# Performance work log

Hardware: AMD Instinct MI355X
Metric: run time of the kernel (lower is better)

The kernel has to match this reference:

```python
import jax, jax.numpy as jnp
import numpy as np

SEQ_LEN = 96
D_MODEL = 512
BATCH = 512
FREQ = SEQ_LEN // 2 + 1  # 49
EPS = 1e-5


def setup_inputs() -> dict:
    key = jax.random.key(0)
    ks = jax.random.split(key, 9)
    s = 1.0 / np.sqrt(D_MODEL)
    return {
        "x": jax.random.normal(ks[0], (BATCH, SEQ_LEN, D_MODEL), jnp.float32),
        "freq_weights": jnp.ones((FREQ,), jnp.float32),
        "Wl": jax.random.normal(ks[1], (D_MODEL, D_MODEL), jnp.float32) * s,
        "bl": jax.random.normal(ks[2], (D_MODEL,), jnp.float32) * s,
        "Wh": jax.random.normal(ks[3], (D_MODEL, D_MODEL), jnp.float32) * s,
        "bh": jax.random.normal(ks[4], (D_MODEL,), jnp.float32) * s,
        "Wg": jax.random.normal(ks[5], (2 * D_MODEL, D_MODEL), jnp.float32) * s,
        "bg": jax.random.normal(ks[6], (D_MODEL,), jnp.float32) * s,
        "gamma": jnp.ones((D_MODEL,), jnp.float32),
        "beta": jnp.zeros((D_MODEL,), jnp.float32),
    }


def reference(x, freq_weights, Wl, bl, Wh, bh, Wg, bg, gamma, beta):
    # Batched rfft over seq axis for all channels at once: [B, F, D] complex
    xf = jnp.fft.rfft(x, axis=1)
    xw = xf * freq_weights[None, :, None]
    cutoff = FREQ // 3  # 16 (static)
    idx = jnp.arange(FREQ)[None, :, None]
    x_low_f = jnp.where(idx < cutoff, xw, 0)
    x_high_f = jnp.where(idx >= cutoff, xw, 0)
    x_low = jnp.fft.irfft(x_low_f, n=SEQ_LEN, axis=1)   # [B, S, D]
    x_high = jnp.fft.irfft(x_high_f, n=SEQ_LEN, axis=1)
    x_low = jnp.einsum("bsd,de->bse", x_low, Wl) + bl
    x_high = jnp.einsum("bsd,de->bse", x_high, Wh) + bh
    gate_in = jnp.concatenate([x_low, x_high], axis=-1)  # [B, S, 2D]
    gate = jax.nn.sigmoid(jnp.einsum("bsd,de->bse", gate_in, Wg) + bg)
    out = gate * x_low + (1.0 - gate) * x_high
    y = x + out  # dropout is identity in eval mode
    mu = jnp.mean(y, axis=-1, keepdims=True)
    var = jnp.var(y, axis=-1, keepdims=True)
    return (y - mu) / jnp.sqrt(var + EPS) * gamma + beta
```

## Files before the change

kernel.cpp:

```cpp
#include <hip/hip_runtime.h>

typedef unsigned short u16;
typedef unsigned int u32;

#define SEQ 96
#define DM 512
#define NBATCH 512
#define NFREQ 49
#define CUT 16
#define MROWS (NBATCH * SEQ)

typedef __attribute__((ext_vector_type(8))) short bf16x8;
typedef __attribute__((ext_vector_type(8))) unsigned short u16x8;
typedef __attribute__((ext_vector_type(4))) float f32x4;

__device__ __forceinline__ u16 f2bf(float f) {
  u32 u = __float_as_uint(f);
  u32 r = (u + 0x7fffu + ((u >> 16) & 1u)) >> 16;
  return (u16)r;
}
__device__ __forceinline__ float bf2f(u16 u) {
  return __uint_as_float(((u32)u) << 16);
}

__device__ __forceinline__ void g2l16(const void* g, void* l) {
  __builtin_amdgcn_global_load_lds(
      (const __attribute__((address_space(1))) void*)g,
      (__attribute__((address_space(3))) void*)l, 16, 0, 0);
}

__global__ void build_filters_k(const float* __restrict__ w,
                                u16* __restrict__ FlB, u16* __restrict__ FhB) {
  int idx = blockIdx.x * 256 + threadIdx.x;
  if (idx >= SEQ * SEQ) return;
  int s = idx / SEQ, t = idx % SEQ;
  int d = s - t;
  const float scale = 1.0f / (float)SEQ;
  const float w0 = 6.283185307179586f / (float)SEQ;
  float cl = 0.f, ch = 0.f;
  for (int k = 0; k < NFREQ; k++) {
    int m = (k * d) % SEQ;
    if (m < 0) m += SEQ;
    float c = (k == 0 || k == SEQ / 2) ? 1.0f : 2.0f;
    float v = c * w[k] * cosf(w0 * (float)m) * scale;
    if (k < CUT) cl += v; else ch += v;
  }
  FlB[idx] = f2bf(cl);
  FhB[idx] = f2bf(ch);
}

__global__ void __launch_bounds__(256) transpose_w_k(
    const float* __restrict__ W, u16* __restrict__ Wt, int K, int N) {
  __shared__ float t[32][33];
  int k0 = blockIdx.x * 32, n0 = blockIdx.y * 32;
  int tx = threadIdx.x & 31, ty = threadIdx.x >> 5;
  #pragma unroll
  for (int r = 0; r < 32; r += 8)
    t[ty + r][tx] = W[(size_t)(k0 + ty + r) * N + n0 + tx];
  __syncthreads();
  #pragma unroll
  for (int r = 0; r < 32; r += 8)
    Wt[(size_t)(n0 + ty + r) * K + k0 + tx] = f2bf(t[tx][ty + r]);
}

__global__ void __launch_bounds__(256) filter_fused_k(
    const float* __restrict__ x, const u16* __restrict__ FlB,
    const u16* __restrict__ FhB, u16* __restrict__ xl, u16* __restrict__ xh) {
  __shared__ __align__(16) u16 Bs[128 * SEQ];
  __shared__ __align__(16) u16 As0[2 * SEQ * SEQ];
  __shared__ float xs[SEQ * 33];
  int tid = threadIdx.x;
  int lane = tid & 63, w = tid >> 6;
  int b = blockIdx.x, d0 = blockIdx.y * 128;

  #pragma unroll
  for (int it = 0; it < 9; it++) {
    int c = it * 256 + tid;
    const u16* src = (c < 1152) ? (FlB + c * 8) : (FhB + (c - 1152) * 8);
    g2l16(src, (char*)As0 + ((it * 256 + w * 64) << 4));
  }

  const float* xb = x + (size_t)b * SEQ * DM + d0;
  u32* BsW = (u32*)Bs;
  #pragma unroll
  for (int q = 0; q < 4; q++) {
    #pragma unroll
    for (int v = 0; v < 3; v++) {
      int c = v * 256 + tid;
      int t = c >> 3, f = (c & 7) << 2;
      float4 fv = *(const float4*)(xb + (size_t)t * DM + q * 32 + f);
      xs[t * 33 + f + 0] = fv.x;
      xs[t * 33 + f + 1] = fv.y;
      xs[t * 33 + f + 2] = fv.z;
      xs[t * 33 + f + 3] = fv.w;
    }
    __syncthreads();
    #pragma unroll
    for (int v = 0; v < 6; v++) {
      int c = v * 256 + tid;
      int dl = c / 48, tw = c % 48;
      u32 lo = (u32)f2bf(xs[(2 * tw) * 33 + dl]);
      u32 hi = (u32)f2bf(xs[(2 * tw + 1) * 33 + dl]);
      BsW[(size_t)(q * 32 + dl) * 48 + tw] = lo | (hi << 16);
    }
    __syncthreads();
  }

  const int l15 = lane & 15, lq = lane >> 4;
  f32x4 acc[2][6][2] = {};
  #pragma unroll
  for (int ks = 0; ks < 3; ks++) {
    int kt = ks * 32;
    bf16x8 bfr[2];
    #pragma unroll
    for (int j = 0; j < 2; j++)
      bfr[j] = *(const bf16x8*)&Bs[(w * 32 + j * 16 + l15) * SEQ + kt + lq * 8];
    #pragma unroll
    for (int f = 0; f < 2; f++)
      #pragma unroll
      for (int i = 0; i < 6; i++) {
        bf16x8 afr = *(const bf16x8*)&As0[f * SEQ * SEQ + (i * 16 + l15) * SEQ + kt + lq * 8];
        #pragma unroll
        for (int j = 0; j < 2; j++)
          acc[f][i][j] = __builtin_amdgcn_mfma_f32_16x16x32_bf16(afr, bfr[j], acc[f][i][j], 0, 0, 0);
      }
  }
  #pragma unroll
  for (int f = 0; f < 2; f++) {
    u16* dst = f ? xh : xl;
    #pragma unroll
    for (int i = 0; i < 6; i++)
      #pragma unroll
      for (int j = 0; j < 2; j++) {
        int d = d0 + w * 32 + j * 16 + l15;
        #pragma unroll
        for (int r = 0; r < 4; r++) {
          int s = i * 16 + lq * 4 + r;
          dst[((size_t)b * SEQ + s) * DM + d] = f2bf(acc[f][i][j][r]);
        }
      }
  }
}

__global__ void __launch_bounds__(256) gemm_proj_mfma_k(
    const u16* __restrict__ xl, const u16* __restrict__ xh,
    const u16* __restrict__ Wlt, const u16* __restrict__ Wht,
    const float* __restrict__ bl, const float* __restrict__ bh,
    u16* __restrict__ yl, u16* __restrict__ yh) {
  const u16* A = blockIdx.z ? xh : xl;
  const u16* Bt = blockIdx.z ? Wht : Wlt;
  const float* bias = blockIdx.z ? bh : bl;
  u16* C = blockIdx.z ? yh : yl;

  __shared__ __align__(16) u16 As[128 * 32];
  __shared__ __align__(16) u16 Bs[128 * 32];
  const int m0 = blockIdx.x * 128;
  const int n0 = blockIdx.y * 128;
  const int tid = threadIdx.x;
  const int lane = tid & 63;
  const int w = tid >> 6;
  const int wm = w & 1, wn = w >> 1;
  const int l15 = lane & 15;
  const int lq = lane >> 4;

  f32x4 acc[4][4] = {};

  for (int kt = 0; kt < 512; kt += 32) {
    #pragma unroll
    for (int r = 0; r < 2; r++) {
      int chunk = r * 256 + tid;
      int row = chunk >> 2;
      int ce = (chunk & 3) << 3;
      u32 lo = (u32)((r * 256 + w * 64) << 4);
      g2l16(A + (size_t)(m0 + row) * 512 + kt + ce, (char*)As + lo);
      g2l16(Bt + (size_t)(n0 + row) * 512 + kt + ce, (char*)Bs + lo);
    }
    __syncthreads();
    bf16x8 af[4], bf[4];
    #pragma unroll
    for (int i = 0; i < 4; i++)
      af[i] = *(const bf16x8*)&As[(wm * 64 + i * 16 + l15) * 32 + lq * 8];
    #pragma unroll
    for (int j = 0; j < 4; j++)
      bf[j] = *(const bf16x8*)&Bs[(wn * 64 + j * 16 + l15) * 32 + lq * 8];
    #pragma unroll
    for (int i = 0; i < 4; i++)
      #pragma unroll
      for (int j = 0; j < 4; j++)
        acc[i][j] = __builtin_amdgcn_mfma_f32_16x16x32_bf16(af[i], bf[j], acc[i][j], 0, 0, 0);
    __syncthreads();
  }

  #pragma unroll
  for (int j = 0; j < 4; j++) {
    int n = n0 + wn * 64 + j * 16 + l15;
    float bv = bias[n];
    #pragma unroll
    for (int i = 0; i < 4; i++) {
      int mrow = m0 + wm * 64 + i * 16 + lq * 4;
      #pragma unroll
      for (int r = 0; r < 4; r++)
        C[(size_t)(mrow + r) * 512 + n] = f2bf(acc[i][j][r] + bv);
    }
  }
}

__global__ void __launch_bounds__(256) gemm_gate_mfma_k(
    const u16* __restrict__ yl, const u16* __restrict__ yh,
    const u16* __restrict__ Wgt, const float* __restrict__ bg,
    u16* __restrict__ g) {
  __shared__ __align__(16) u16 As[128 * 32];
  __shared__ __align__(16) u16 Bs[128 * 32];
  const int m0 = blockIdx.x * 128;
  const int n0 = blockIdx.y * 128;
  const int tid = threadIdx.x;
  const int lane = tid & 63;
  const int w = tid >> 6;
  const int wm = w & 1, wn = w >> 1;
  const int l15 = lane & 15;
  const int lq = lane >> 4;

  f32x4 acc[4][4] = {};

  for (int kt = 0; kt < 1024; kt += 32) {
    const u16* Ak = (kt < 512) ? yl : yh;
    int ka = kt & 511;
    #pragma unroll
    for (int r = 0; r < 2; r++) {
      int chunk = r * 256 + tid;
      int row = chunk >> 2;
      int ce = (chunk & 3) << 3;
      u32 lo = (u32)((r * 256 + w * 64) << 4);
      g2l16(Ak + (size_t)(m0 + row) * 512 + ka + ce, (char*)As + lo);
      g2l16(Wgt + (size_t)(n0 + row) * 1024 + kt + ce, (char*)Bs + lo);
    }
    __syncthreads();
    bf16x8 af[4], bf[4];
    #pragma unroll
    for (int i = 0; i < 4; i++)
      af[i] = *(const bf16x8*)&As[(wm * 64 + i * 16 + l15) * 32 + lq * 8];
    #pragma unroll
    for (int j = 0; j < 4; j++)
      bf[j] = *(const bf16x8*)&Bs[(wn * 64 + j * 16 + l15) * 32 + lq * 8];
    #pragma unroll
    for (int i = 0; i < 4; i++)
      #pragma unroll
      for (int j = 0; j < 4; j++)
        acc[i][j] = __builtin_amdgcn_mfma_f32_16x16x32_bf16(af[i], bf[j], acc[i][j], 0, 0, 0);
    __syncthreads();
  }

  #pragma unroll
  for (int j = 0; j < 4; j++) {
    int n = n0 + wn * 64 + j * 16 + l15;
    float bv = bg[n];
    #pragma unroll
    for (int i = 0; i < 4; i++) {
      int mrow = m0 + wm * 64 + i * 16 + lq * 4;
      #pragma unroll
      for (int r = 0; r < 4; r++) {
        float z = acc[i][j][r] + bv;
        g[(size_t)(mrow + r) * 512 + n] = f2bf(1.0f / (1.0f + __expf(-z)));
      }
    }
  }
}

__global__ void __launch_bounds__(256) final_ln_k(
    const float* __restrict__ x, const u16* __restrict__ yl,
    const u16* __restrict__ yh, const u16* __restrict__ g,
    const float* __restrict__ gamma, const float* __restrict__ beta,
    float* __restrict__ out) {
  const int wave = threadIdx.x >> 6;
  const int lane = threadIdx.x & 63;
  const size_t row = (size_t)blockIdx.x * 4 + wave;
  const size_t base = row * 512 + lane * 8;
  const int e = lane * 8;

  float4 xv0 = *(const float4*)(x + base);
  float4 xv1 = *(const float4*)(x + base + 4);
  u16x8 lv = *(const u16x8*)(yl + base);
  u16x8 hv = *(const u16x8*)(yh + base);
  u16x8 gv = *(const u16x8*)(g + base);

  float v[8];
  const float xs[8] = {xv0.x, xv0.y, xv0.z, xv0.w, xv1.x, xv1.y, xv1.z, xv1.w};
  float sum = 0.f, sumsq = 0.f;
  #pragma unroll
  for (int k = 0; k < 8; k++) {
    float gl = bf2f(gv[k]);
    float vv = xs[k] + gl * bf2f(lv[k]) + (1.f - gl) * bf2f(hv[k]);
    v[k] = vv;
    sum += vv;
    sumsq += vv * vv;
  }
  #pragma unroll
  for (int off = 32; off; off >>= 1) {
    sum += __shfl_xor(sum, off);
    sumsq += __shfl_xor(sumsq, off);
  }
  const float mu = sum * (1.f / 512.f);
  const float var = sumsq * (1.f / 512.f) - mu * mu;
  const float inv = rsqrtf(var + 1e-5f);

  float4 gm0 = *(const float4*)(gamma + e);
  float4 gm1 = *(const float4*)(gamma + e + 4);
  float4 bt0 = *(const float4*)(beta + e);
  float4 bt1 = *(const float4*)(beta + e + 4);
  float4 o0, o1;
  o0.x = (v[0] - mu) * inv * gm0.x + bt0.x;
  o0.y = (v[1] - mu) * inv * gm0.y + bt0.y;
  o0.z = (v[2] - mu) * inv * gm0.z + bt0.z;
  o0.w = (v[3] - mu) * inv * gm0.w + bt0.w;
  o1.x = (v[4] - mu) * inv * gm1.x + bt1.x;
  o1.y = (v[5] - mu) * inv * gm1.y + bt1.y;
  o1.z = (v[6] - mu) * inv * gm1.z + bt1.z;
  o1.w = (v[7] - mu) * inv * gm1.w + bt1.w;
  *(float4*)(out + base) = o0;
  *(float4*)(out + base + 4) = o1;
}

extern "C" void kernel_launch(void* const* d_in, const int* in_sizes, int n_in,
                              void* d_out, int out_size, void* d_ws, size_t ws_size,
                              hipStream_t stream) {
  const float* x     = (const float*)d_in[0];
  const float* fw    = (const float*)d_in[1];
  const float* Wl    = (const float*)d_in[2];
  const float* bl    = (const float*)d_in[3];
  const float* Wh    = (const float*)d_in[4];
  const float* bh    = (const float*)d_in[5];
  const float* Wg    = (const float*)d_in[6];
  const float* bg    = (const float*)d_in[7];
  const float* gamma = (const float*)d_in[8];
  const float* beta  = (const float*)d_in[9];
  float* out = (float*)d_out;

  char* ws = (char*)d_ws;
  u16* FlB = (u16*)ws;
  u16* FhB = FlB + SEQ * SEQ;
  u16* Wlt = (u16*)(ws + 64 * 1024);
  u16* Wht = Wlt + 512 * 512;
  u16* Wgt = Wht + 512 * 512;
  size_t tsz = (size_t)MROWS * 512;
  u16* xl = (u16*)(ws + 4 * 1024 * 1024);
  u16* xh = xl + tsz;
  u16* yl = xh + tsz;
  u16* yh = yl + tsz;
  u16* gbuf = xl;

  build_filters_k<<<dim3(36), dim3(256), 0, stream>>>(fw, FlB, FhB);
  transpose_w_k<<<dim3(16, 16), dim3(256), 0, stream>>>(Wl, Wlt, 512, 512);
  transpose_w_k<<<dim3(16, 16), dim3(256), 0, stream>>>(Wh, Wht, 512, 512);
  transpose_w_k<<<dim3(32, 16), dim3(256), 0, stream>>>(Wg, Wgt, 1024, 512);
  filter_fused_k<<<dim3(NBATCH, DM / 128), dim3(256), 0, stream>>>(x, FlB, FhB, xl, xh);
  gemm_proj_mfma_k<<<dim3(MROWS / 128, 4, 2), dim3(256), 0, stream>>>(
      xl, xh, Wlt, Wht, bl, bh, yl, yh);
  gemm_gate_mfma_k<<<dim3(MROWS / 128, 4), dim3(256), 0, stream>>>(yl, yh, Wgt, bg, gbuf);
  final_ln_k<<<dim3(MROWS / 4), dim3(256), 0, stream>>>(x, yl, yh, gbuf, gamma, beta, out);
}
```

Before: 441.5 us.

## Fold projection weights into gate weights and fuse projection and gate GEMMs

Precomputes a combined gate weight Wgc = [Wl·Wg_top; Wh·Wg_bot] and a combined bias b2, so the gate pre-activation can be computed directly from xl/xh instead of from yl/yh. A single 512-thread kernel then runs two groups of waves over the same A tiles: one group produces yl and yh, the other produces the sigmoid gate. This drops the separate gate GEMM and its re-read of yl/yh, and shares the A loads across both. In exchange it adds small weight-prep kernels, extra workspace, a K=1024 loop per block, and extra bf16 rounding in the composed weights. The fused path only runs when the workspace is large enough, otherwise the old two-GEMM path is kept.

Result: slower. 571.8 us (+29.5%).

```diff
diff --git a/kernel.cpp b/kernel.cpp
--- a/kernel.cpp
+++ b/kernel.cpp
@@ -50,17 +50,92 @@
 }
 
 __global__ void __launch_bounds__(256) transpose_w_k(
-    const float* __restrict__ W, u16* __restrict__ Wt, int K, int N) {
+    const float* __restrict__ W, u16* __restrict__ Wt, int K, int N,
+    u16* __restrict__ WB) {
   __shared__ float t[32][33];
   int k0 = blockIdx.x * 32, n0 = blockIdx.y * 32;
   int tx = threadIdx.x & 31, ty = threadIdx.x >> 5;
   #pragma unroll
-  for (int r = 0; r < 32; r += 8)
-    t[ty + r][tx] = W[(size_t)(k0 + ty + r) * N + n0 + tx];
+  for (int r = 0; r < 32; r += 8) {
+    float v = W[(size_t)(k0 + ty + r) * N + n0 + tx];
+    t[ty + r][tx] = v;
+    if (WB) WB[(size_t)(k0 + ty + r) * N + n0 + tx] = f2bf(v);
+  }
   __syncthreads();
   #pragma unroll
   for (int r = 0; r < 32; r += 8)
     Wt[(size_t)(n0 + ty + r) * K + k0 + tx] = f2bf(t[tx][ty + r]);
+}
+
+__global__ void __launch_bounds__(256) wgc_build_k(
+    const u16* __restrict__ Wgt, const u16* __restrict__ WlB,
+    const u16* __restrict__ WhB, u16* __restrict__ Wgc) {
+  __shared__ __align__(16) u16 As[128 * 32];
+  __shared__ __align__(16) u16 Bs[128 * 32];
+  const int n0 = blockIdx.x * 128;
+  const int k0 = blockIdx.y * 128;
+  const int zoff = blockIdx.z ? 512 : 0;
+  const u16* WB = blockIdx.z ? WhB : WlB;
+  const int tid = threadIdx.x;
+  const int lane = tid & 63;
+  const int w = tid >> 6;
+  const int wm = w & 1, wn = w >> 1;
+  const int l15 = lane & 15;
+  const int lq = lane >> 4;
+
+  f32x4 acc[4][4] = {};
+
+  for (int kt = 0; kt < 512; kt += 32) {
+    #pragma unroll
+    for (int r = 0; r < 2; r++) {
+      int chunk = r * 256 + tid;
+      int row = chunk >> 2;
+      int ce = (chunk & 3) << 3;
+      u32 lo = (u32)((r * 256 + w * 64) << 4);
+      g2l16(Wgt + (size_t)(n0 + row) * 1024 + zoff + kt + ce, (char*)As + lo);
+      g2l16(WB + (size_t)(k0 + row) * 512 + kt + ce, (char*)Bs + lo);
+    }
+    __syncthreads();
+    bf16x8 af[4], bf[4];
+    #pragma unroll
+    for (int i = 0; i < 4; i++)
+      af[i] = *(const bf16x8*)&As[(wm * 64 + i * 16 + l15) * 32 + lq * 8];
+    #pragma unroll
+    for (int j = 0; j < 4; j++)
+      bf[j] = *(const bf16x8*)&Bs[(wn * 64 + j * 16 + l15) * 32 + lq * 8];
+    #pragma unroll
+    for (int i = 0; i < 4; i++)
+      #pragma unroll
+      for (int j = 0; j < 4; j++)
+        acc[i][j] = __builtin_amdgcn_mfma_f32_16x16x32_bf16(af[i], bf[j], acc[i][j], 0, 0, 0);
+    __syncthreads();
+  }
+
+  #pragma unroll
+  for (int j = 0; j < 4; j++) {
+    int kcol = k0 + wn * 64 + j * 16 + l15;
+    #pragma unroll
+    for (int i = 0; i < 4; i++) {
+      int nrow = n0 + wm * 64 + i * 16 + lq * 4;
+      #pragma unroll
+      for (int r = 0; r < 4; r++)
+        Wgc[(size_t)(nrow + r) * 1024 + zoff + kcol] = f2bf(acc[i][j][r]);
+    }
+  }
+}
+
+__global__ void __launch_bounds__(256) b2_k(
+    const float* __restrict__ Wg, const float* __restrict__ bl,
+    const float* __restrict__ bh, const float* __restrict__ bg,
+    float* __restrict__ b2) {
+  int n = blockIdx.x * 256 + threadIdx.x;
+  float s = bg[n];
+  #pragma unroll 4
+  for (int e = 0; e < 512; e++) {
+    s += bl[e] * Wg[(size_t)e * 512 + n];
+    s += bh[e] * Wg[(size_t)(512 + e) * 512 + n];
+  }
+  b2[n] = s;
 }
 
 __global__ void __launch_bounds__(256) filter_fused_k(
@@ -139,6 +214,104 @@
           dst[((size_t)b * SEQ + s) * DM + d] = f2bf(acc[f][i][j][r]);
         }
       }
+  }
+}
+
+__global__ void __launch_bounds__(512) fused_pg_k(
+    const u16* __restrict__ xl, const u16* __restrict__ xh,
+    const u16* __restrict__ Wlt, const u16* __restrict__ Wht,
+    const u16* __restrict__ Wgc,
+    const float* __restrict__ bl, const float* __restrict__ bh,
+    const float* __restrict__ b2,
+    u16* __restrict__ yl, u16* __restrict__ yh, u16* __restrict__ g) {
+  __shared__ __align__(16) u16 As[128 * 32];
+  __shared__ __align__(16) u16 By[128 * 32];
+  __shared__ __align__(16) u16 Bz[128 * 32];
+  const int m0 = blockIdx.x * 128;
+  const int n0 = blockIdx.y * 128;
+  const int tid = threadIdx.x;
+  const int lane = tid & 63;
+  const int w = tid >> 6;
+  const bool isY = (w < 4);
+  const int wz = w & 3;
+  const int wm = wz & 1, wn = wz >> 1;
+  const int l15 = lane & 15;
+  const int lq = lane >> 4;
+  const f32x4 fzero = {0.f, 0.f, 0.f, 0.f};
+
+  const int rowS = tid >> 2;
+  const int ce = (tid & 3) << 3;
+  const u32 ldsoff = (u32)((w * 64) << 4);
+
+  f32x4 acc[4][4] = {};
+
+  for (int kt = 0; kt < 1024; kt += 32) {
+    const u16* Asrc = (kt < 512) ? xl : xh;
+    const u16* Bysrc = (kt < 512) ? Wlt : Wht;
+    const int ka = kt & 511;
+    g2l16(Asrc + (size_t)(m0 + rowS) * 512 + ka + ce, (char*)As + ldsoff);
+    g2l16(Bysrc + (size_t)(n0 + rowS) * 512 + ka + ce, (char*)By + ldsoff);
+    g2l16(Wgc + (size_t)(n0 + rowS) * 1024 + kt + ce, (char*)Bz + ldsoff);
+    __syncthreads();
+    const u16* Bsel = isY ? By : Bz;
+    bf16x8 af[4], bf[4];
+    #pragma unroll
+    for (int i = 0; i < 4; i++)
+      af[i] = *(const bf16x8*)&As[(wm * 64 + i * 16 + l15) * 32 + lq * 8];
+    #pragma unroll
+    for (int j = 0; j < 4; j++)
+      bf[j] = *(const bf16x8*)&Bsel[(wn * 64 + j * 16 + l15) * 32 + lq * 8];
+    #pragma unroll
+    for (int i = 0; i < 4; i++)
+      #pragma unroll
+      for (int j = 0; j < 4; j++)
+        acc[i][j] = __builtin_amdgcn_mfma_f32_16x16x32_bf16(af[i], bf[j], acc[i][j], 0, 0, 0);
+    if (kt == 480 && isY) {
+      #pragma unroll
+      for (int j = 0; j < 4; j++) {
+        int n = n0 + wn * 64 + j * 16 + l15;
+        float bv = bl[n];
+        #pragma unroll
+        for (int i = 0; i < 4; i++) {
+          int mrow = m0 + wm * 64 + i * 16 + lq * 4;
+          #pragma unroll
+          for (int r = 0; r < 4; r++)
+            yl[(size_t)(mrow + r) * 512 + n] = f2bf(acc[i][j][r] + bv);
+          acc[i][j] = fzero;
+        }
+      }
+    }
+    __syncthreads();
+  }
+
+  if (isY) {
+    #pragma unroll
+    for (int j = 0; j < 4; j++) {
+      int n = n0 + wn * 64 + j * 16 + l15;
+      float bv = bh[n];
+      #pragma unroll
+      for (int i = 0; i < 4; i++) {
+        int mrow = m0 + wm * 64 + i * 16 + lq * 4;
+        #pragma unroll
+        for (int r = 0; r < 4; r++)
+          yh[(size_t)(mrow + r) * 512 + n] = f2bf(acc[i][j][r] + bv);
+      }
+    }
+  } else {
+    #pragma unroll
+    for (int j = 0; j < 4; j++) {
+      int n = n0 + wn * 64 + j * 16 + l15;
+      float bv = b2[n];
+      #pragma unroll
+      for (int i = 0; i < 4; i++) {
+        int mrow = m0 + wm * 64 + i * 16 + lq * 4;
+        #pragma unroll
+        for (int r = 0; r < 4; r++) {
+          float z = acc[i][j][r] + bv;
+          g[(size_t)(mrow + r) * 512 + n] = f2bf(1.0f / (1.0f + __expf(-z)));
+        }
+      }
+    }
   }
 }
 
@@ -341,20 +514,38 @@
   u16* Wlt = (u16*)(ws + 64 * 1024);
   u16* Wht = Wlt + 512 * 512;
   u16* Wgt = Wht + 512 * 512;
+  u16* WlB = Wgt + 512 * 1024;
+  u16* WhB = WlB + 512 * 512;
+  u16* Wgc = WhB + 512 * 512;
+  float* b2 = (float*)(ws + 6 * 1024 * 1024);
   size_t tsz = (size_t)MROWS * 512;
-  u16* xl = (u16*)(ws + 4 * 1024 * 1024);
+  u16* xl = (u16*)(ws + 8 * 1024 * 1024);
   u16* xh = xl + tsz;
   u16* yl = xh + tsz;
   u16* yh = yl + tsz;
-  u16* gbuf = xl;
+
+  const bool fused = ws_size >= (size_t)8 * 1024 * 1024 + 5 * tsz * sizeof(u16);
+  u16* gbuf = fused ? (yh + tsz) : xl;
 
   build_filters_k<<<dim3(36), dim3(256), 0, stream>>>(fw, FlB, FhB);
-  transpose_w_k<<<dim3(16, 16), dim3(256), 0, stream>>>(Wl, Wlt, 512, 512);
-  transpose_w_k<<<dim3(16, 16), dim3(256), 0, stream>>>(Wh, Wht, 512, 512);
-  transpose_w_k<<<dim3(32, 16), dim3(256), 0, stream>>>(Wg, Wgt, 1024, 512);
+  transpose_w_k<<<dim3(16, 16), dim3(256), 0, stream>>>(Wl, Wlt, 512, 512,
+                                                        fused ? WlB : nullptr);
+  transpose_w_k<<<dim3(16, 16), dim3(256), 0, stream>>>(Wh, Wht, 512, 512,
+                                                        fused ? WhB : nullptr);
+  transpose_w_k<<<dim3(32, 16), dim3(256), 0, stream>>>(Wg, Wgt, 1024, 512, nullptr);
   filter_fused_k<<<dim3(NBATCH, DM / 128), dim3(256), 0, stream>>>(x, FlB, FhB, xl, xh);
-  gemm_proj_mfma_k<<<dim3(MROWS / 128, 4, 2), dim3(256), 0, stream>>>(
-      xl, xh, Wlt, Wht, bl, bh, yl, yh);
-  gemm_gate_mfma_k<<<dim3(MROWS / 128, 4), dim3(256), 0, stream>>>(yl, yh, Wgt, bg, gbuf);
-  final_ln_k<<<dim3(MROWS / 4), dim3(256), 0, stream>>>(x, yl, yh, gbuf, gamma, beta, out);
-}
+
+  if (fused) {
+    wgc_build_k<<<dim3(4, 4, 2), dim3(256), 0, stream>>>(Wgt, WlB, WhB, Wgc);
+    b2_k<<<dim3(2), dim3(256), 0, stream>>>(Wg, bl, bh, bg, b2);
+    fused_pg_k<<<dim3(MROWS / 128, 4), dim3(512), 0, stream>>>(
+        xl, xh, Wlt, Wht, Wgc, bl, bh, b2, yl, yh, gbuf);
+  } else {
+    gemm_proj_mfma_k<<<dim3(MROWS / 128, 4, 2), dim3(256), 0, stream>>>(
+        xl, xh, Wlt, Wht, bl, bh, yl, yh);
+    gemm_gate_mfma_k<<<dim3(MROWS / 128, 4), dim3(256), 0, stream>>>(
+        yl, yh, Wgt, bg, gbuf);
+  }
+  final_ln_k<<<dim3(MROWS / 4), dim3(256), 0, stream>>>(
+      x, yl, yh, gbuf, gamma, beta, out);
+}
```
